# Optimization experiments

Measured on AMD Instinct MI355X. Metric: run time of the kernel, lower is better.

The kernel has to match this reference:

```python
import jax, jax.numpy as jnp
import numpy as np

N_NODES = 100000
DIM_IN = 128
DIM_H = 64
LATENT = 64
N_EDGES = 1200000


def setup_inputs() -> dict:
    key = jax.random.key(0)
    ks = jax.random.split(key, 8)
    x = jax.random.normal(ks[0], (N_NODES, DIM_IN), dtype=jnp.float32)
    edge_index = jax.random.randint(ks[1], (2, N_EDGES), 0, N_NODES, dtype=jnp.int32)
    batch = jnp.zeros((N_NODES,), dtype=jnp.int32)
    s_in = 1.0 / np.sqrt(DIM_IN)
    s_h = 1.0 / np.sqrt(DIM_H)
    gcn_w = jax.random.uniform(ks[2], (DIM_IN, DIM_H), jnp.float32, -s_in, s_in)
    gcn_b = jnp.zeros((DIM_H,), dtype=jnp.float32)
    w1 = jax.random.uniform(ks[3], (DIM_H, LATENT), jnp.float32, -s_h, s_h)
    b1 = jax.random.uniform(ks[4], (LATENT,), jnp.float32, -s_h, s_h)
    s_l = 1.0 / np.sqrt(LATENT)
    w3 = jax.random.uniform(ks[5], (LATENT, LATENT), jnp.float32, -s_l, s_l)
    b3 = jax.random.uniform(ks[6], (LATENT,), jnp.float32, -s_l, s_l)
    return {"x": x, "edge_index": edge_index, "batch": batch,
            "gcn_w": gcn_w, "gcn_b": gcn_b, "w1": w1, "b1": b1, "w3": w3, "b3": b3}


def _gcn_conv(x, edge_index, W, b):
    n = x.shape[0]
    loop = jnp.arange(n, dtype=edge_index.dtype)
    src = jnp.concatenate([edge_index[0], loop])
    dst = jnp.concatenate([edge_index[1], loop])
    deg = jax.ops.segment_sum(jnp.ones_like(dst, dtype=x.dtype), dst, num_segments=n)
    dinv = jnp.where(deg > 0, jax.lax.rsqrt(deg), 0.0)
    norm = dinv[src] * dinv[dst]                      # [E+N]
    h = x @ W                                          # [N, dim_h]
    msg = h[src] * norm[:, None]                       # gather + scale
    out = jax.ops.segment_sum(msg, dst, num_segments=n)  # scatter-add
    return out + b


def reference(x, edge_index, batch, gcn_w, gcn_b, w1, b1, w3, b3):
    g1 = _gcn_conv(x, edge_index, gcn_w, gcn_b)
    l1 = g1 @ w1 + b1
    l3 = l1 @ w3 + b3
    # mu/sigma/z/kl in the original are side effects not returned; output is l3
    return l3
```

## Files before the change

kernel.cpp:

```cpp
#include <hip/hip_runtime.h>
#include <hip/hip_bf16.h>

#define N_NODES 100000
#define N_EDGES 1200000
#define NBK 256
#define NPB 391
#define CAPB 5376
#define EPB 4096
#define BIN_BLKS 293
#define XW_BLKS 1280
#define FUSED_GRID (BIN_BLKS + XW_BLKS)
#define GB 2048

typedef __attribute__((ext_vector_type(8))) short bf16x8;
typedef __attribute__((ext_vector_type(4))) float f32x4;

__global__ __launch_bounds__(256) void k_w(const float* __restrict__ gcn_w,
                                           const float* __restrict__ gcn_b,
                                           const float* __restrict__ w1,
                                           const float* __restrict__ b1,
                                           const float* __restrict__ w3,
                                           const float* __restrict__ b3,
                                           short* __restrict__ WcB,
                                           float* __restrict__ bc,
                                           int* __restrict__ bcnt) {
    __shared__ float tmp[4096];
    __shared__ float tb[64];
    const int b = blockIdx.x, t = threadIdx.x;
    if (b == 31 && t < NBK) bcnt[t] = 0;
    if (b == 0 && t < 64) {
        float s = b1[t];
        for (int k = 0; k < 64; ++k) s = fmaf(gcn_b[k], w1[k * 64 + t], s);
        tb[t] = s;
    }
    for (int i = t; i < 4096; i += 256) {
        const int r = i >> 6, c = i & 63;
        float a = 0.f;
#pragma unroll 8
        for (int k = 0; k < 64; ++k) a = fmaf(w1[r * 64 + k], w3[k * 64 + c], a);
        tmp[i] = a;
    }
    __syncthreads();
    const int i = b * 256 + t;
    const int r = i >> 6, c = i & 63;
    float a = 0.f;
#pragma unroll 8
    for (int k = 0; k < 64; ++k) a = fmaf(gcn_w[r * 64 + k], tmp[k * 64 + c], a);
    const int kt = r >> 5, kr = r & 31, g = kr >> 3, e = kr & 7;
    const int ct = c & 3, cl = c >> 2, lane = g * 16 + cl;
    WcB[(((kt * 4 + ct) * 64) + lane) * 8 + e] =
        __builtin_bit_cast(short, __float2bfloat16(a));
    if (b == 0 && t < 64) {
        float s = b3[t];
        for (int k = 0; k < 64; ++k) s = fmaf(tb[k], w3[k * 64 + t], s);
        bc[t] = s;
    }
}

__global__ __launch_bounds__(256) void k_fused(const int* __restrict__ ei,
                                               int* __restrict__ bcnt,
                                               int* __restrict__ binned,
                                               const float* __restrict__ x,
                                               const short* __restrict__ WcB,
                                               unsigned char* __restrict__ hsq,
                                               float* __restrict__ hscale) {
    const int b = blockIdx.x;
    if (b < BIN_BLKS) {
        __shared__ int hist[NBK], base[NBK], cur[NBK];
        const int t = threadIdx.x;
        const int e0 = b * EPB;
        for (int i = t; i < NBK; i += 256) hist[i] = 0;
        __syncthreads();
        for (int j = t; j < EPB; j += 256) {
            const int e = e0 + j;
            if (e < N_EDGES) atomicAdd(&hist[ei[N_EDGES + e] / NPB], 1);
        }
        __syncthreads();
        for (int i = t; i < NBK; i += 256) {
            const int h = hist[i];
            base[i] = h ? atomicAdd(&bcnt[i], h) : 0;
            cur[i] = 0;
        }
        __syncthreads();
        for (int j = t; j < EPB; j += 256) {
            const int e = e0 + j;
            if (e < N_EDGES) {
                const int s = ei[e];
                const int d = ei[N_EDGES + e];
                const int bk = d / NPB;
                const int dl = d - bk * NPB;
                const int p = base[bk] + atomicAdd(&cur[bk], 1);
                if (p < CAPB) binned[bk * CAPB + p] = s | (dl << 17);
            }
        }
    } else {
        const int t = threadIdx.x, w = t >> 6, lane = t & 63;
        const int cl = lane & 15, g = lane >> 4;
        bf16x8 bfrag[16];
#pragma unroll
        for (int f = 0; f < 16; ++f) bfrag[f] = ((const bf16x8*)WcB)[f * 64 + lane];

        const int ntiles = N_NODES / 16;
        const int nw = XW_BLKS * 4;
        for (int tile = (b - BIN_BLKS) * 4 + w; tile < ntiles; tile += nw) {
            const int node0 = tile * 16;
            const float* xrow = x + (size_t)(node0 + cl) * 128 + g * 8;
            f32x4 xa[4][2];
#pragma unroll
            for (int kt = 0; kt < 4; ++kt) {
                xa[kt][0] = *(const f32x4*)(xrow + kt * 32);
                xa[kt][1] = *(const f32x4*)(xrow + kt * 32 + 4);
            }
            f32x4 acc[4];
#pragma unroll
            for (int ct = 0; ct < 4; ++ct) acc[ct] = (f32x4){0.f, 0.f, 0.f, 0.f};
#pragma unroll
            for (int kt = 0; kt < 4; ++kt) {
                bf16x8 af;
#pragma unroll
                for (int j = 0; j < 4; ++j) {
                    af[j]     = __builtin_bit_cast(short, __float2bfloat16(xa[kt][0][j]));
                    af[j + 4] = __builtin_bit_cast(short, __float2bfloat16(xa[kt][1][j]));
                }
#pragma unroll
                for (int ct = 0; ct < 4; ++ct)
                    acc[ct] = __builtin_amdgcn_mfma_f32_16x16x32_bf16(
                        af, bfrag[kt * 4 + ct], acc[ct], 0, 0, 0);
            }
            float mx[4];
#pragma unroll
            for (int j = 0; j < 4; ++j) {
                mx[j] = fmaxf(fmaxf(fabsf(acc[0][j]), fabsf(acc[1][j])),
                              fmaxf(fabsf(acc[2][j]), fabsf(acc[3][j])));
            }
#pragma unroll
            for (int m = 1; m < 16; m <<= 1)
#pragma unroll
                for (int j = 0; j < 4; ++j)
                    mx[j] = fmaxf(mx[j], __shfl_xor(mx[j], m));
#pragma unroll
            for (int j = 0; j < 4; ++j) {
                const float sc = fmaxf(mx[j], 1e-20f) * (1.f / 127.f);
                const float inv = 127.f / fmaxf(mx[j], 1e-20f);
                unsigned int pk = 0;
#pragma unroll
                for (int ct = 0; ct < 4; ++ct) {
                    const int v = (int)rintf(acc[ct][j] * inv);
                    pk |= ((unsigned int)(v & 0xFF)) << (8 * ct);
                }
                *(unsigned int*)(hsq + (size_t)(node0 + g * 4 + j) * 64 + cl * 4) = pk;
                if (cl == j) hscale[node0 + g * 4 + j] = sc;
            }
        }
    }
}

__global__ __launch_bounds__(512) void k_csr(const int* __restrict__ bcnt,
                                             const int* __restrict__ binned,
                                             const float* __restrict__ hscale,
                                             int* __restrict__ csr,
                                             int* __restrict__ rowptr,
                                             int* __restrict__ degA,
                                             float* __restrict__ dinv,
                                             float* __restrict__ csca) {
    __shared__ int stage[CAPB];
    __shared__ int sdeg[NPB], sloc[NPB], scur[NPB];
    const int b = blockIdx.x, t = threadIdx.x;
    const int m = min(bcnt[b], CAPB);
    for (int i = t; i < NPB; i += 512) { sdeg[i] = 0; scur[i] = 0; }
    __syncthreads();
    for (int j = t; j < m; j += 512) {
        const int pk = binned[b * CAPB + j];
        stage[j] = pk;
        atomicAdd(&sdeg[pk >> 17], 1);
    }
    __syncthreads();
    if (t < 64) {
        int run = 0;
#pragma unroll
        for (int c0 = 0; c0 < NPB; c0 += 64) {
            const int idx = c0 + t;
            const int v = (idx < NPB) ? sdeg[idx] : 0;
            int inc = v;
#pragma unroll
            for (int o = 1; o < 64; o <<= 1) {
                const int u = __shfl_up(inc, o);
                if (t >= o) inc += u;
            }
            if (idx < NPB) sloc[idx] = run + inc - v;
            run += __shfl(inc, 63);
        }
    }
    __syncthreads();
    for (int i = t; i < NPB; i += 512) {
        const int node = b * NPB + i;
        if (node < N_NODES) {
            const int v = sdeg[i];
            const float dv = rsqrtf((float)(v + 1));
            rowptr[node] = b * CAPB + sloc[i];
            degA[node] = v;
            dinv[node] = dv;
            csca[node] = dv * hscale[node];
        }
    }
    for (int j = t; j < m; j += 512) {
        const int pk = stage[j];
        const int dl = pk >> 17;
        const int p = atomicAdd(&scur[dl], 1);
        csr[b * CAPB + sloc[dl] + p] = pk & 0x1FFFF;
    }
}

__global__ __launch_bounds__(256) void k_gather(const int* __restrict__ rowptr,
                                                const int* __restrict__ degA,
                                                const int* __restrict__ csr,
                                                const unsigned char* __restrict__ hsq,
                                                const float* __restrict__ csca,
                                                const float* __restrict__ dinv,
                                                const float* __restrict__ bc,
                                                float* __restrict__ out) {
    const int t = threadIdx.x, wv = t >> 6, lane = t & 63;
    const int cl = lane & 15, g = lane >> 4, cc = cl * 4;
    const int NW = GB * 4;
    int n = blockIdx.x * 4 + wv;
    const float4 bc4 = *(const float4*)(bc + cc);

    int deg0 = degA[n], base0 = rowptr[n];
    float dvn0 = dinv[n], csn0 = csca[n];
    unsigned qs0 = *(const unsigned*)(hsq + (size_t)n * 64 + cc);
    int s0 = 0; float c0 = 0.f;
    {
        const int r = min(deg0, 64);
        if (lane < r) { s0 = csr[base0 + lane]; c0 = csca[s0]; }
    }
    int n1 = n + NW;
    int deg1 = 0, base1 = 0; float dvn1 = 0.f, csn1 = 0.f; unsigned qs1 = 0;
    if (n1 < N_NODES) {
        deg1 = degA[n1]; base1 = rowptr[n1];
        dvn1 = dinv[n1]; csn1 = csca[n1];
        qs1 = *(const unsigned*)(hsq + (size_t)n1 * 64 + cc);
    }

    for (;;) {
        const int r1 = min(deg1, 64);
        int s1 = 0;
        if (n1 < N_NODES && lane < r1) s1 = csr[base1 + lane];
        const int n2 = n1 + NW;
        int deg2 = 0, base2 = 0; float dvn2 = 0.f, csn2 = 0.f; unsigned qs2 = 0;
        if (n2 < N_NODES) {
            deg2 = degA[n2]; base2 = rowptr[n2];
            dvn2 = dinv[n2]; csn2 = csca[n2];
            qs2 = *(const unsigned*)(hsq + (size_t)n2 * 64 + cc);
        }
        f32x4 acc = (f32x4){0.f, 0.f, 0.f, 0.f};
        const int r0 = min(deg0, 64);
        for (int i0 = 0; i0 < r0; i0 += 16) {
#pragma unroll
            for (int u = 0; u < 4; ++u) {
                const int jj = i0 + u * 4 + g;
                const int sj = __shfl(s0, jj);
                const float cj = __shfl(c0, jj);
                if (jj < r0) {
                    const unsigned q = *(const unsigned*)(hsq + (size_t)sj * 64 + cc);
                    acc[0] = fmaf((float)(int)(signed char)(q & 0xFFu), cj, acc[0]);
                    acc[1] = fmaf((float)(int)(signed char)((q >> 8) & 0xFFu), cj, acc[1]);
                    acc[2] = fmaf((float)(int)(signed char)((q >> 16) & 0xFFu), cj, acc[2]);
                    acc[3] = fmaf((float)(int)(signed char)(q >> 24), cj, acc[3]);
                }
            }
        }
        for (int j0 = 64; j0 < deg0; j0 += 64) {
            const int rem = min(deg0 - j0, 64);
            int sl = 0; float clv = 0.f;
            if (lane < rem) { sl = csr[base0 + j0 + lane]; clv = csca[sl]; }
            for (int i0 = 0; i0 < rem; i0 += 16) {
#pragma unroll
                for (int u = 0; u < 4; ++u) {
                    const int jj = i0 + u * 4 + g;
                    const int sj = __shfl(sl, jj);
                    const float cj = __shfl(clv, jj);
                    if (jj < rem) {
                        const unsigned q = *(const unsigned*)(hsq + (size_t)sj * 64 + cc);
                        acc[0] = fmaf((float)(int)(signed char)(q & 0xFFu), cj, acc[0]);
                        acc[1] = fmaf((float)(int)(signed char)((q >> 8) & 0xFFu), cj, acc[1]);
                        acc[2] = fmaf((float)(int)(signed char)((q >> 16) & 0xFFu), cj, acc[2]);
                        acc[3] = fmaf((float)(int)(signed char)(q >> 24), cj, acc[3]);
                    }
                }
            }
        }
#pragma unroll
        for (int k = 0; k < 4; ++k) {
            acc[k] += __shfl_xor(acc[k], 16);
            acc[k] += __shfl_xor(acc[k], 32);
        }
        float4 res;
        res.x = fmaf(fmaf((float)(int)(signed char)(qs0 & 0xFFu), csn0, acc[0]), dvn0, bc4.x);
        res.y = fmaf(fmaf((float)(int)(signed char)((qs0 >> 8) & 0xFFu), csn0, acc[1]), dvn0, bc4.y);
        res.z = fmaf(fmaf((float)(int)(signed char)((qs0 >> 16) & 0xFFu), csn0, acc[2]), dvn0, bc4.z);
        res.w = fmaf(fmaf((float)(int)(signed char)(qs0 >> 24), csn0, acc[3]), dvn0, bc4.w);
        if (g == 0) *(float4*)(out + (size_t)n * 64 + cc) = res;

        if (n1 >= N_NODES) break;
        float c1 = 0.f;
        if (lane < r1) c1 = csca[s1];
        n = n1; deg0 = deg1; base0 = base1; dvn0 = dvn1; csn0 = csn1;
        qs0 = qs1; s0 = s1; c0 = c1;
        n1 = n2; deg1 = deg2; base1 = base2; dvn1 = dvn2; csn1 = csn2; qs1 = qs2;
    }
}

extern "C" void kernel_launch(void* const* d_in, const int* in_sizes, int n_in,
                              void* d_out, int out_size, void* d_ws, size_t ws_size,
                              hipStream_t stream) {
    const float* x     = (const float*)d_in[0];
    const int*   ei    = (const int*)d_in[1];
    const float* gcn_w = (const float*)d_in[3];
    const float* gcn_b = (const float*)d_in[4];
    const float* w1    = (const float*)d_in[5];
    const float* b1    = (const float*)d_in[6];
    const float* w3    = (const float*)d_in[7];
    const float* b3    = (const float*)d_in[8];
    float* out = (float*)d_out;

    char* ws = (char*)d_ws;
    int*           bcnt   = (int*)(ws);
    short*         WcB    = (short*)(ws + 1024);
    float*         bc     = (float*)(ws + 17408);
    float*         dinv   = (float*)(ws + 17664);
    int*           rowptr = (int*)(ws + 417664);
    int*           degA   = (int*)(ws + 817664);
    float*         hscale = (float*)(ws + 1217664);
    float*         csca   = (float*)(ws + 1617664);
    unsigned char* hsq    = (unsigned char*)(ws + 2017664);
    int*           binned = (int*)(ws + 8417664);
    int*           csr    = (int*)(ws + 13922688);

    k_w<<<32, 256, 0, stream>>>(gcn_w, gcn_b, w1, b1, w3, b3, WcB, bc, bcnt);
    k_fused<<<FUSED_GRID, 256, 0, stream>>>(ei, bcnt, binned, x, WcB, hsq, hscale);
    k_csr<<<NBK, 512, 0, stream>>>(bcnt, binned, hscale, csr, rowptr, degA, dinv, csca);
    k_gather<<<GB, 256, 0, stream>>>(rowptr, degA, csr, hsq, csca, dinv, bc, out);
}
```

Before: 102.3 us.

## Split bucket counters and bins per XCD to localize atomics and writes

The edge-binning stage now keeps a separate counter and sub-bin per bucket for each XCD, selected by reading the hardware XCC ID, so global atomics and scattered stores stay within one die's L2 instead of crossing dies. The CSR build kernel then concatenates the eight sub-bins into shared memory before counting degrees. This adds an extra pass and sync in k_csr and enlarges the binned workspace. It also caps each sub-bin at a fixed capacity, so a skewed XCD distribution could overflow a sub-bin and silently drop edges.

```diff
diff --git a/kernel.cpp b/kernel.cpp
--- a/kernel.cpp
+++ b/kernel.cpp
@@ -5,6 +5,8 @@
 #define N_EDGES 1200000
 #define NBK 256
 #define NPB 391
+#define NSUB 8
+#define CAPS 2048
 #define CAPB 5376
 #define EPB 4096
 #define BIN_BLKS 293
@@ -23,11 +25,12 @@
                                            const float* __restrict__ b3,
                                            short* __restrict__ WcB,
                                            float* __restrict__ bc,
-                                           int* __restrict__ bcnt) {
+                                           int* __restrict__ bcnt8) {
     __shared__ float tmp[4096];
     __shared__ float tb[64];
     const int b = blockIdx.x, t = threadIdx.x;
-    if (b == 31 && t < NBK) bcnt[t] = 0;
+    if (b == 31)
+        for (int i = t; i < NBK * NSUB; i += 256) bcnt8[i] = 0;
     if (b == 0 && t < 64) {
         float s = b1[t];
         for (int k = 0; k < 64; ++k) s = fmaf(gcn_b[k], w1[k * 64 + t], s);
@@ -58,7 +61,7 @@
 }
 
 __global__ __launch_bounds__(256) void k_fused(const int* __restrict__ ei,
-                                               int* __restrict__ bcnt,
+                                               int* __restrict__ bcnt8,
                                                int* __restrict__ binned,
                                                const float* __restrict__ x,
                                                const short* __restrict__ WcB,
@@ -69,6 +72,9 @@
         __shared__ int hist[NBK], base[NBK], cur[NBK];
         const int t = threadIdx.x;
         const int e0 = b * EPB;
+        unsigned xcd;
+        asm volatile("s_getreg_b32 %0, hwreg(HW_REG_XCC_ID)" : "=s"(xcd));
+        xcd &= 7;
         for (int i = t; i < NBK; i += 256) hist[i] = 0;
         __syncthreads();
         for (int j = t; j < EPB; j += 256) {
@@ -78,7 +84,7 @@
         __syncthreads();
         for (int i = t; i < NBK; i += 256) {
             const int h = hist[i];
-            base[i] = h ? atomicAdd(&bcnt[i], h) : 0;
+            base[i] = h ? atomicAdd(&bcnt8[i * NSUB + xcd], h) : 0;
             cur[i] = 0;
         }
         __syncthreads();
@@ -90,7 +96,8 @@
                 const int bk = d / NPB;
                 const int dl = d - bk * NPB;
                 const int p = base[bk] + atomicAdd(&cur[bk], 1);
-                if (p < CAPB) binned[bk * CAPB + p] = s | (dl << 17);
+                if (p < CAPS)
+                    binned[((size_t)(bk * NSUB + xcd)) * CAPS + p] = s | (dl << 17);
             }
         }
     } else {
@@ -155,7 +162,7 @@
     }
 }
 
-__global__ __launch_bounds__(512) void k_csr(const int* __restrict__ bcnt,
+__global__ __launch_bounds__(512) void k_csr(const int* __restrict__ bcnt8,
                                              const int* __restrict__ binned,
                                              const float* __restrict__ hscale,
                                              int* __restrict__ csr,
@@ -165,15 +172,29 @@
                                              float* __restrict__ csca) {
     __shared__ int stage[CAPB];
     __shared__ int sdeg[NPB], sloc[NPB], scur[NPB];
+    __shared__ int soff[NSUB + 1];
     const int b = blockIdx.x, t = threadIdx.x;
-    const int m = min(bcnt[b], CAPB);
+    if (t == 0) {
+        int o = 0;
+#pragma unroll
+        for (int k = 0; k < NSUB; ++k) {
+            soff[k] = o;
+            const int c = min(bcnt8[b * NSUB + k], CAPS);
+            o = min(o + c, CAPB);
+        }
+        soff[NSUB] = o;
+    }
     for (int i = t; i < NPB; i += 512) { sdeg[i] = 0; scur[i] = 0; }
     __syncthreads();
-    for (int j = t; j < m; j += 512) {
-        const int pk = binned[b * CAPB + j];
-        stage[j] = pk;
-        atomicAdd(&sdeg[pk >> 17], 1);
-    }
+    const int m = soff[NSUB];
+#pragma unroll
+    for (int k = 0; k < NSUB; ++k) {
+        const int n = soff[k + 1] - soff[k];
+        for (int j = t; j < n; j += 512)
+            stage[soff[k] + j] = binned[((size_t)(b * NSUB + k)) * CAPS + j];
+    }
+    __syncthreads();
+    for (int j = t; j < m; j += 512) atomicAdd(&sdeg[stage[j] >> 17], 1);
     __syncthreads();
     if (t < 64) {
         int run = 0;
@@ -324,20 +345,20 @@
     float* out = (float*)d_out;
 
     char* ws = (char*)d_ws;
-    int*           bcnt   = (int*)(ws);
-    short*         WcB    = (short*)(ws + 1024);
-    float*         bc     = (float*)(ws + 17408);
-    float*         dinv   = (float*)(ws + 17664);
-    int*           rowptr = (int*)(ws + 417664);
-    int*           degA   = (int*)(ws + 817664);
-    float*         hscale = (float*)(ws + 1217664);
-    float*         csca   = (float*)(ws + 1617664);
-    unsigned char* hsq    = (unsigned char*)(ws + 2017664);
-    int*           binned = (int*)(ws + 8417664);
-    int*           csr    = (int*)(ws + 13922688);
-
-    k_w<<<32, 256, 0, stream>>>(gcn_w, gcn_b, w1, b1, w3, b3, WcB, bc, bcnt);
-    k_fused<<<FUSED_GRID, 256, 0, stream>>>(ei, bcnt, binned, x, WcB, hsq, hscale);
-    k_csr<<<NBK, 512, 0, stream>>>(bcnt, binned, hscale, csr, rowptr, degA, dinv, csca);
+    int*           bcnt8  = (int*)(ws);
+    short*         WcB    = (short*)(ws + 8192);
+    float*         bc     = (float*)(ws + 24576);
+    float*         dinv   = (float*)(ws + 24832);
+    int*           rowptr = (int*)(ws + 424832);
+    int*           degA   = (int*)(ws + 824832);
+    float*         hscale = (float*)(ws + 1224832);
+    float*         csca   = (float*)(ws + 1624832);
+    unsigned char* hsq    = (unsigned char*)(ws + 2024832);
+    int*           binned = (int*)(ws + 8424832);
+    int*           csr    = (int*)(ws + 25202048);
+
+    k_w<<<32, 256, 0, stream>>>(gcn_w, gcn_b, w1, b1, w3, b3, WcB, bc, bcnt8);
+    k_fused<<<FUSED_GRID, 256, 0, stream>>>(ei, bcnt8, binned, x, WcB, hsq, hscale);
+    k_csr<<<NBK, 512, 0, stream>>>(bcnt8, binned, hscale, csr, rowptr, degA, dinv, csca);
     k_gather<<<GB, 256, 0, stream>>>(rowptr, degA, csr, hsq, csca, dinv, bc, out);
 }
```

Result: slower. 105.2 us (+2.8%).
